# Optimization experiments

Hardware: AMD Instinct MI355X
Metric: run time of the kernel (lower is better)

The kernel has to match this reference:

```python
import jax, jax.numpy as jnp
import numpy as np

N_NODES = 100000
N_EDGES = 1600000
N_GRAPHS = 256
HIDDEN = 128
IN_FEAT = 5


def setup_inputs() -> dict:
    key = jax.random.key(0)
    ks = jax.random.split(key, 12)
    x = jax.random.normal(ks[0], (N_NODES, IN_FEAT), dtype=jnp.float32)
    edge_index = jax.random.randint(ks[1], (2, N_EDGES), 0, N_NODES, dtype=jnp.int64)
    batch = jnp.sort(jax.random.randint(ks[2], (N_NODES,), 0, N_GRAPHS, dtype=jnp.int64))
    s = 0.05
    W0 = jax.random.normal(ks[3], (IN_FEAT, HIDDEN), dtype=jnp.float32) * s
    b0 = jnp.zeros((HIDDEN,), dtype=jnp.float32)
    W1 = jax.random.normal(ks[4], (HIDDEN, HIDDEN), dtype=jnp.float32) * s
    b1 = jnp.zeros((HIDDEN,), dtype=jnp.float32)
    W2 = jax.random.normal(ks[5], (HIDDEN, HIDDEN), dtype=jnp.float32) * s
    b2 = jnp.zeros((HIDDEN,), dtype=jnp.float32)
    lin_w = jax.random.normal(ks[6], (HIDDEN, 1), dtype=jnp.float32) * s
    lin_b = jnp.zeros((1,), dtype=jnp.float32)
    return {"x": x, "edge_index": edge_index, "batch": batch,
            "W0": W0, "b0": b0, "W1": W1, "b1": b1, "W2": W2, "b2": b2,
            "lin_w": lin_w, "lin_b": lin_b}


def reference(x, edge_index, batch, W0, b0, W1, b1, W2, b2, lin_w, lin_b):
    n = x.shape[0]
    # PyG GCNConv: add self-loops, symmetric normalization D^-1/2 (A+I) D^-1/2
    loop = jnp.arange(n, dtype=edge_index.dtype)
    src = jnp.concatenate([edge_index[0], loop])  # [E+N]
    dst = jnp.concatenate([edge_index[1], loop])
    deg = jax.ops.segment_sum(jnp.ones_like(dst, dtype=x.dtype), dst, num_segments=n)
    dis = jnp.where(deg > 0, jax.lax.rsqrt(jnp.maximum(deg, 1.0)), 0.0)
    norm = (dis[src] * dis[dst])[:, None]  # [E+N, 1]

    def gcn_conv(h, W, b):
        h = h @ W                      # [N, H]
        msg = h[src] * norm            # gather + scale, [E+N, H]
        return jax.ops.segment_sum(msg, dst, num_segments=n) + b

    h = jax.nn.relu(gcn_conv(x, W0, b0))
    h = jax.nn.relu(gcn_conv(h, W1, b1))
    h = gcn_conv(h, W2, b2)

    # global_mean_pool over batch ids
    sums = jax.ops.segment_sum(h, batch, num_segments=N_GRAPHS)
    cnt = jax.ops.segment_sum(jnp.ones((n,), x.dtype), batch, num_segments=N_GRAPHS)
    g = sums / jnp.maximum(cnt, 1.0)[:, None]
    # dropout p=0.01 is identity in eval mode
    return jax.nn.sigmoid(g @ lin_w + lin_b)  # [N_GRAPHS, 1]
```

## Files before the change

### kernel.cpp

```cpp
#include <hip/hip_runtime.h>
#include <hip/hip_fp8.h>

#define GCN_N 100000
#define GCN_H 128
#define GCN_G 256
#define NPB_SHIFT 9
#define NPB 512
#define NBKT 196
#define CHUNK 2048
#define SRC_BITS 17
#define SRC_MASK ((1 << SRC_BITS) - 1)
#define T1_SCALE 256.0f
#define T1_INV_SCALE (1.0f / 256.0f)
#define EBUF_CAP 10240

static_assert(GCN_N < (1 << SRC_BITS), "src id must fit 17 bits");

using short8 = __attribute__((ext_vector_type(8))) short;
using f32x4  = __attribute__((ext_vector_type(4))) float;
using f32x2  = __attribute__((ext_vector_type(2))) float;

#if defined(__has_builtin)
#if __has_builtin(__builtin_amdgcn_cvt_pk_f32_fp8) && __has_builtin(__builtin_amdgcn_cvt_pk_fp8_f32)
#define HW_FP8 1
#endif
#endif


__device__ __forceinline__ unsigned short f2bf(float f) {
    unsigned u = __float_as_uint(f);
    unsigned r = u + 0x7FFFu + ((u >> 16) & 1u);
    return (unsigned short)(r >> 16);
}
__device__ __forceinline__ float bf2f(unsigned short h) {
    return __uint_as_float(((unsigned)h) << 16);
}

__device__ __forceinline__ void fp8x4_to_f32(unsigned v, float* f) {
#ifdef HW_FP8
    f32x2 lo = __builtin_amdgcn_cvt_pk_f32_fp8((int)v, false);
    f32x2 hi = __builtin_amdgcn_cvt_pk_f32_fp8((int)v, true);
    f[0] = lo[0]; f[1] = lo[1]; f[2] = hi[0]; f[3] = hi[1];
#else
    #pragma unroll
    for (int j = 0; j < 4; j++) {
        __hip_fp8_e4m3 h;
        h.__x = (unsigned char)((v >> (8 * j)) & 0xFF);
        f[j] = (float)h;
    }
#endif
}

__device__ __forceinline__ unsigned f32x4_to_fp8(float f0, float f1, float f2, float f3) {
#ifdef HW_FP8
    int r = __builtin_amdgcn_cvt_pk_fp8_f32(f0, f1, 0, false);
    r = __builtin_amdgcn_cvt_pk_fp8_f32(f2, f3, r, true);
    return (unsigned)r;
#else
    unsigned r = 0;
    float ff[4] = {f0, f1, f2, f3};
    #pragma unroll
    for (int j = 0; j < 4; j++) {
        __hip_fp8_e4m3 h(ff[j]);
        r |= ((unsigned)h.__x) << (8 * j);
    }
    return r;
#endif
}


__global__ __launch_bounds__(256) void hist_kernel(const int* __restrict__ dst,
                                                   int* __restrict__ hist, int E) {
    __shared__ int lh[NBKT];
    int tid = threadIdx.x;
    if (tid < NBKT) lh[tid] = 0;
    __syncthreads();
    int e0 = blockIdx.x * CHUNK;
    #pragma unroll
    for (int i = 0; i < CHUNK / 256; i++) {
        int e = e0 + tid + i * 256;
        if (e < E) atomicAdd(&lh[dst[e] >> NPB_SHIFT], 1);
    }
    __syncthreads();
    if (tid < NBKT) hist[(size_t)blockIdx.x * NBKT + tid] = lh[tid];
}

__global__ __launch_bounds__(64) void scan_cols_kernel(const int* __restrict__ hist,
                                                       int* __restrict__ offsT,
                                                       int* __restrict__ btot, int B) {
    int k = blockIdx.x;
    int lane = threadIdx.x;
    int running = 0;
    for (int b0 = 0; b0 < B; b0 += 64) {
        int b = b0 + lane;
        int v = (b < B) ? hist[(size_t)b * NBKT + k] : 0;
        int iv = v;
        #pragma unroll
        for (int d = 1; d < 64; d <<= 1) {
            int x = __shfl_up(iv, d, 64);
            if (lane >= d) iv += x;
        }
        if (b < B) offsT[(size_t)k * B + b] = running + iv - v;
        running += __shfl(iv, 63, 64);
    }
    if (lane == 0) btot[k] = running;
}

__global__ __launch_bounds__(256) void prep_kernel(const float* __restrict__ W1,
                                                   const float* __restrict__ W2,
                                                   const float* __restrict__ b2,
                                                   const float* __restrict__ lw,
                                                   const int* __restrict__ btot,
                                                   unsigned short* __restrict__ w1t,
                                                   float* __restrict__ w2l,
                                                   float* __restrict__ c2,
                                                   int* __restrict__ bbase,
                                                   int* __restrict__ rowptr, int n) {
    __shared__ float slw[128];
    int blk = blockIdx.x, tid = threadIdx.x;
    if (blk < 64) {
        int idx = blk * 256 + tid;
        int col = idx >> 7, k = idx & 127;
        w1t[idx] = f2bf(W1[k * 128 + col]);
    } else if (blk == 64) {
        if (tid < 128) slw[tid] = lw[tid];
        __syncthreads();
        if (tid < 128) {
            float s = 0.f;
            #pragma unroll 8
            for (int j = 0; j < 128; j++) s = fmaf(W2[tid * 128 + j], slw[j], s);
            w2l[tid] = s;
        } else if (tid == 128) {
            float s = 0.f;
            for (int j = 0; j < 128; j++) s = fmaf(b2[j], slw[j], s);
            c2[0] = s;
        }
    } else {
        if (tid == 0) {
            int run = 0;
            for (int i = 0; i < NBKT; i++) { bbase[i] = run; run += btot[i]; }
            bbase[NBKT] = run;
            rowptr[n] = run;
        }
    }
}

__global__ __launch_bounds__(256) void partition_kernel(const int* __restrict__ src,
                                                        const int* __restrict__ dst,
                                                        const int* __restrict__ bbase,
                                                        const int* __restrict__ offsT,
                                                        int* __restrict__ epack,
                                                        int E, int B) {
    __shared__ int cur[NBKT];
    int blk = blockIdx.x, tid = threadIdx.x;
    if (tid < NBKT) cur[tid] = bbase[tid] + offsT[(size_t)tid * B + blk];
    __syncthreads();
    int e0 = blk * CHUNK;
    #pragma unroll
    for (int i = 0; i < CHUNK / 256; i++) {
        int e = e0 + tid + i * 256;
        if (e < E) {
            int d = dst[e];
            int s = src[e];
            int pos = atomicAdd(&cur[d >> NPB_SHIFT], 1);
            epack[pos] = ((d & (NPB - 1)) << SRC_BITS) | s;
        }
    }
}

__global__ __launch_bounds__(512) void csr_build_kernel(const int* __restrict__ epack,
                                                        const int* __restrict__ bbase,
                                                        const float* __restrict__ x,
                                                        int* __restrict__ rowptr,
                                                        float* __restrict__ dis,
                                                        float* __restrict__ xsp,
                                                        int* __restrict__ csrc, int n) {
    __shared__ int ebuf[EBUF_CAP];
    __shared__ int lcount[NPB];
    __shared__ int lcur[NPB];
    __shared__ int wsums[8];
    int k = blockIdx.x, tid = threadIdx.x;
    int lane = tid & 63, wid = tid >> 6;
    int nodebase = k << NPB_SHIFT;
    int ebeg = bbase[k], eend = bbase[k + 1];
    bool fits = (eend - ebeg) <= EBUF_CAP;

    lcount[tid] = 0;
    __syncthreads();
    for (int e = ebeg + tid; e < eend; e += 512) {
        int p = epack[e];
        if (fits) ebuf[e - ebeg] = p;
        atomicAdd(&lcount[p >> SRC_BITS], 1);
    }
    __syncthreads();

    int v = lcount[tid];
    int iv = v;
    #pragma unroll
    for (int d = 1; d < 64; d <<= 1) {
        int x2 = __shfl_up(iv, d, 64);
        if (lane >= d) iv += x2;
    }
    if (lane == 63) wsums[wid] = iv;
    __syncthreads();
    if (tid == 0) {
        int r = 0;
        #pragma unroll
        for (int w = 0; w < 8; w++) { int t = wsums[w]; wsums[w] = r; r += t; }
    }
    __syncthreads();
    int ex = wsums[wid] + iv - v;
    lcur[tid] = ex;
    int node = nodebase + tid;
    if (node < n) {
        rowptr[node] = ebeg + ex;
        float dd = rsqrtf((float)(v + 1));
        dis[node] = dd;
        const float* xr = x + (size_t)node * 5;
        float4 a;
        a.x = xr[0] * dd; a.y = xr[1] * dd; a.z = xr[2] * dd; a.w = xr[3] * dd;
        float a4 = xr[4] * dd;
        ((float4*)(xsp + (size_t)node * 8))[0] = a;
        xsp[(size_t)node * 8 + 4] = a4;
        xsp[(size_t)node * 8 + 5] = 0.f;
        xsp[(size_t)node * 8 + 6] = 0.f;
        xsp[(size_t)node * 8 + 7] = 0.f;
    }
    __syncthreads();
    for (int e = ebeg + tid; e < eend; e += 512) {
        int p = fits ? ebuf[e - ebeg] : epack[e];
        int pos = atomicAdd(&lcur[p >> SRC_BITS], 1);
        csrc[ebeg + pos] = p & SRC_MASK;
    }
}


__global__ __launch_bounds__(256) void aggx_kernel(const float* __restrict__ xsp,
                                                   const float* __restrict__ dis,
                                                   const int* __restrict__ rowptr,
                                                   const int* __restrict__ csrc,
                                                   float* __restrict__ a0p, int n) {
    int i = blockIdx.x * 256 + threadIdx.x;
    if (i >= n) return;
    float4 acc = ((const float4*)(xsp + (size_t)i * 8))[0];
    float acc4 = xsp[(size_t)i * 8 + 4];
    int r0 = rowptr[i], r1 = rowptr[i + 1];
    int e = r0;
    for (; e + 7 < r1; e += 8) {
        int ss[8];
        #pragma unroll
        for (int u = 0; u < 8; u++) ss[u] = csrc[e + u];
        float4 v[8]; float a4[8];
        #pragma unroll
        for (int u = 0; u < 8; u++) {
            v[u] = ((const float4*)(xsp + (size_t)ss[u] * 8))[0];
            a4[u] = xsp[(size_t)ss[u] * 8 + 4];
        }
        #pragma unroll
        for (int u = 0; u < 8; u++) {
            acc.x += v[u].x; acc.y += v[u].y; acc.z += v[u].z; acc.w += v[u].w;
            acc4 += a4[u];
        }
    }
    for (; e < r1; e++) {
        int s = csrc[e];
        float4 v = ((const float4*)(xsp + (size_t)s * 8))[0];
        acc.x += v.x; acc.y += v.y; acc.z += v.z; acc.w += v.w;
        acc4 += xsp[(size_t)s * 8 + 4];
    }
    float di = dis[i];
    acc.x *= di; acc.y *= di; acc.z *= di; acc.w *= di; acc4 *= di;
    ((float4*)(a0p + (size_t)i * 8))[0] = acc;
    a0p[(size_t)i * 8 + 4] = acc4;
}


__global__ __launch_bounds__(256) void mmfused_kernel(const float* __restrict__ a0p,
                                                      const float* __restrict__ W0,
                                                      const float* __restrict__ b0,
                                                      const unsigned short* __restrict__ w1t,
                                                      const float* __restrict__ dis,
                                                      unsigned* __restrict__ t1f8, int n) {
    __shared__ __align__(16) unsigned short sA[128 * 128];
    __shared__ __align__(16) unsigned short sBT[128 * 128];
    __shared__ __align__(16) float4 sA0[256];
    __shared__ float sDis[128];
    char* sAb = (char*)sA;
    char* sBb = (char*)sBT;
    int tid = threadIdx.x;
    int rowBase = blockIdx.x * 128;

    {
        int rowL = tid >> 1, q = tid & 1;
        int gr = rowBase + rowL;
        float4 v = make_float4(0.f, 0.f, 0.f, 0.f);
        if (gr < n) v = ((const float4*)a0p)[(size_t)gr * 2 + q];
        sA0[tid] = v;
        if (tid < 128) {
            int g2 = rowBase + tid;
            sDis[tid] = (g2 < n) ? dis[g2] : 0.f;
        }
    }
    #pragma unroll
    for (int it = 0; it < 8; it++) {
        int idx = tid + it * 256;
        int col = idx >> 4, c = idx & 15;
        uint4 v = ((const uint4*)w1t)[idx];
        int byteoff = (col * 256 + c * 16) ^ ((col & 7) << 4);
        *(uint4*)(sBb + byteoff) = v;
    }
    __syncthreads();

    {
        int cq = tid & 31;
        int rg = tid >> 5;
        float4 w0q[5];
        #pragma unroll
        for (int j = 0; j < 5; j++) w0q[j] = *((const float4*)(W0 + j * 128 + cq * 4));
        float4 b0q = *((const float4*)(b0 + cq * 4));
        const float* sA0f = (const float*)sA0;
        #pragma unroll
        for (int ri = 0; ri < 16; ri++) {
            int row = rg + ri * 8;
            const float* ar = sA0f + row * 8;
            float4 h = b0q;
            #pragma unroll
            for (int j = 0; j < 5; j++) {
                float aj = ar[j];
                h.x = fmaf(aj, w0q[j].x, h.x);
                h.y = fmaf(aj, w0q[j].y, h.y);
                h.z = fmaf(aj, w0q[j].z, h.z);
                h.w = fmaf(aj, w0q[j].w, h.w);
            }
            h.x = fmaxf(h.x, 0.f); h.y = fmaxf(h.y, 0.f);
            h.z = fmaxf(h.z, 0.f); h.w = fmaxf(h.w, 0.f);
            uint2 p;
            p.x = (unsigned)f2bf(h.x) | ((unsigned)f2bf(h.y) << 16);
            p.y = (unsigned)f2bf(h.z) | ((unsigned)f2bf(h.w) << 16);
            int byteoff = (row * 256 + cq * 8) ^ ((row & 7) << 4);
            *(uint2*)(sAb + byteoff) = p;
        }
    }
    __syncthreads();

    int wave = tid >> 6, l = tid & 63;
    int lr = l & 15, lg = l >> 4;
    int rb = wave * 32;

    short8 afr[2][4];
    #pragma unroll
    for (int rt = 0; rt < 2; rt++) {
        int row = rb + rt * 16 + lr;
        #pragma unroll
        for (int ks = 0; ks < 4; ks++) {
            int byteoff = (row * 256 + ks * 64 + lg * 16) ^ ((row & 7) << 4);
            afr[rt][ks] = *(const short8*)(sAb + byteoff);
        }
    }
    f32x4 acc[2][8];
    #pragma unroll
    for (int rt = 0; rt < 2; rt++)
        #pragma unroll
        for (int ct = 0; ct < 8; ct++)
            acc[rt][ct] = (f32x4){0.f, 0.f, 0.f, 0.f};

    #pragma unroll
    for (int ct = 0; ct < 8; ct++) {
        int col = ct * 16 + lr;
        short8 bfr[4];
        #pragma unroll
        for (int ks = 0; ks < 4; ks++) {
            int byteoff = (col * 256 + ks * 64 + lg * 16) ^ ((col & 7) << 4);
            bfr[ks] = *(const short8*)(sBb + byteoff);
        }
        #pragma unroll
        for (int rt = 0; rt < 2; rt++) {
            #pragma unroll
            for (int ks = 0; ks < 4; ks++) {
                acc[rt][ct] = __builtin_amdgcn_mfma_f32_16x16x32_bf16(
                    afr[rt][ks], bfr[ks], acc[rt][ct], 0, 0, 0);
            }
        }
    }

    #pragma unroll
    for (int rt = 0; rt < 2; rt++) {
        #pragma unroll
        for (int i = 0; i < 4; i++) {
            int rowL = rb + rt * 16 + lg * 4 + i;
            float dsc = sDis[rowL] * T1_SCALE;
            #pragma unroll
            for (int ct = 0; ct < 8; ct++) {
                int col = ct * 16 + lr;
                int byteoff = (rowL * 256 + col * 2) ^ ((rowL & 7) << 4);
                *(unsigned short*)(sAb + byteoff) = f2bf(acc[rt][ct][i] * dsc);
            }
        }
    }
    __syncthreads();

    #pragma unroll
    for (int it = 0; it < 8; it++) {
        int flat = tid + it * 256;
        int rowL = flat >> 4, c16 = flat & 15;
        int gr = rowBase + rowL;
        if (gr < n) {
            int byteoff = (rowL * 256 + c16 * 16) ^ ((rowL & 7) << 4);
            uint4 v = *(const uint4*)(sAb + byteoff);
            float f0 = __uint_as_float(v.x << 16), f1 = __uint_as_float(v.x & 0xFFFF0000u);
            float f2 = __uint_as_float(v.y << 16), f3 = __uint_as_float(v.y & 0xFFFF0000u);
            float f4 = __uint_as_float(v.z << 16), f5 = __uint_as_float(v.z & 0xFFFF0000u);
            float f6 = __uint_as_float(v.w << 16), f7 = __uint_as_float(v.w & 0xFFFF0000u);
            uint2 p;
            p.x = f32x4_to_fp8(f0, f1, f2, f3);
            p.y = f32x4_to_fp8(f4, f5, f6, f7);
            ((uint2*)t1f8)[(size_t)gr * 16 + c16] = p;
        }
    }
}


__global__ __launch_bounds__(256) void agg1_kernel(const unsigned* __restrict__ t1f8,
                                                   const float* __restrict__ dis,
                                                   const int* __restrict__ rowptr,
                                                   const int* __restrict__ csrc,
                                                   const float* __restrict__ b1,
                                                   const float* __restrict__ w2l,
                                                   float* __restrict__ z, int n) {
    int group = threadIdx.x >> 4, lane = threadIdx.x & 15;
    int i = blockIdx.x * 16 + group;
    if (i >= n) return;
    const uint2* t2 = (const uint2*)t1f8;
    float f[8], acc[8];
    uint2 sv = t2[(size_t)i * 16 + lane];
    fp8x4_to_f32(sv.x, f);
    fp8x4_to_f32(sv.y, f + 4);
    #pragma unroll
    for (int j = 0; j < 8; j++) acc[j] = f[j];
    int r0 = rowptr[i], r1 = rowptr[i + 1];
    for (int e = r0; e < r1; e += 16) {
        int cnt = r1 - e; if (cnt > 16) cnt = 16;
        int idx = e + lane;
        int si = (idx < r1) ? csrc[idx] : 0;
        uint2 vv[16];
        #pragma unroll
        for (int u = 0; u < 16; u++) {
            if (u < cnt) {
                int s = __shfl(si, u, 16);
                vv[u] = t2[(size_t)s * 16 + lane];
            }
        }
        #pragma unroll
        for (int u = 0; u < 16; u++) {
            if (u < cnt) {
                fp8x4_to_f32(vv[u].x, f);
                fp8x4_to_f32(vv[u].y, f + 4);
                #pragma unroll
                for (int j = 0; j < 8; j++) acc[j] += f[j];
            }
        }
    }
    float di = dis[i];
    float dis_s = di * T1_INV_SCALE;
    float4 b4a = ((const float4*)b1)[lane * 2];
    float4 b4b = ((const float4*)b1)[lane * 2 + 1];
    float4 w4a = ((const float4*)w2l)[lane * 2];
    float4 w4b = ((const float4*)w2l)[lane * 2 + 1];
    float bb[8] = {b4a.x, b4a.y, b4a.z, b4a.w, b4b.x, b4b.y, b4b.z, b4b.w};
    float ww[8] = {w4a.x, w4a.y, w4a.z, w4a.w, w4b.x, w4b.y, w4b.z, w4b.w};
    float d = 0.f;
    #pragma unroll
    for (int j = 0; j < 8; j++) {
        float c = fmaxf(fmaf(dis_s, acc[j], bb[j]), 0.f);
        d = fmaf(c, ww[j], d);
    }
    #pragma unroll
    for (int o = 8; o > 0; o >>= 1) d += __shfl_down(d, o, 16);
    if (lane == 0) z[i] = di * d;
}


__global__ __launch_bounds__(256) void aggz_pool_kernel(const float* __restrict__ z,
                                                        const float* __restrict__ dis,
                                                        const int* __restrict__ rowptr,
                                                        const int* __restrict__ csrc,
                                                        const int* __restrict__ batch,
                                                        float* __restrict__ gsum,
                                                        int* __restrict__ gcnt, int n) {
    __shared__ float lg[GCN_G];
    __shared__ int lc[GCN_G];
    int tid = threadIdx.x;
    lg[tid] = 0.f;
    lc[tid] = 0;
    __syncthreads();
    int i = blockIdx.x * 256 + tid;
    bool valid = i < n;
    float ndv = 0.f;
    int g = 0;
    if (valid) {
        float acc = z[i];
        int r0 = rowptr[i], r1 = rowptr[i + 1];
        int e = r0;
        for (; e + 7 < r1; e += 8) {
            int ss[8];
            #pragma unroll
            for (int u = 0; u < 8; u++) ss[u] = csrc[e + u];
            float zv[8];
            #pragma unroll
            for (int u = 0; u < 8; u++) zv[u] = z[ss[u]];
            #pragma unroll
            for (int u = 0; u < 8; u++) acc += zv[u];
        }
        for (; e < r1; e++) acc += z[csrc[e]];
        ndv = dis[i] * acc;
        g = batch[i];
    }
    int lane = tid & 63;
    int g0 = __shfl(g, 0, 64);
    bool uni = __all(g == g0) && __all(valid);
    if (uni) {
        float s = ndv;
        #pragma unroll
        for (int o = 32; o > 0; o >>= 1) s += __shfl_down(s, o, 64);
        if (lane == 0) {
            atomicAdd(&lg[g0], s);
            atomicAdd(&lc[g0], 64);
        }
    } else if (valid) {
        atomicAdd(&lg[g], ndv);
        atomicAdd(&lc[g], 1);
    }
    __syncthreads();
    float v = lg[tid];
    int c = lc[tid];
    if (v != 0.f) atomicAdd(&gsum[tid], v);
    if (c != 0) atomicAdd(&gcnt[tid], c);
}


__global__ __launch_bounds__(256) void final_kernel(const float* __restrict__ gsum,
                                                    const int* __restrict__ gcnt,
                                                    const float* __restrict__ c2,
                                                    const float* __restrict__ lb,
                                                    float* __restrict__ out) {
    int g = threadIdx.x;
    float cnt = (float)max(gcnt[g], 1);
    float v = gsum[g] / cnt + c2[0] + lb[0];
    out[g] = 1.f / (1.f + expf(-v));
}


extern "C" void kernel_launch(void* const* d_in, const int* in_sizes, int n_in,
                              void* d_out, int out_size, void* d_ws, size_t ws_size,
                              hipStream_t stream) {
    const float* x   = (const float*)d_in[0];
    const int*   ei  = (const int*)d_in[1];
    const int*   bat = (const int*)d_in[2];
    const float* W0  = (const float*)d_in[3];
    const float* b0  = (const float*)d_in[4];
    const float* W1  = (const float*)d_in[5];
    const float* b1  = (const float*)d_in[6];
    const float* W2  = (const float*)d_in[7];
    const float* b2  = (const float*)d_in[8];
    const float* lw  = (const float*)d_in[9];
    const float* lb  = (const float*)d_in[10];
    float* out = (float*)d_out;

    const int N = GCN_N;
    const int E = in_sizes[1] / 2;
    const int B = (E + CHUNK - 1) / CHUNK;

    char* ws = (char*)d_ws;
    size_t off = 0;
    auto alloc = [&](size_t bytes) {
        size_t o = off;
        off += (bytes + 255) & ~(size_t)255;
        return o;
    };
    int*   hist    = (int*)(ws + alloc((size_t)B * NBKT * 4));
    int*   offsT   = (int*)(ws + alloc((size_t)NBKT * B * 4));
    int*   btot    = (int*)(ws + alloc((size_t)NBKT * 4));
    int*   bbase   = (int*)(ws + alloc((size_t)(NBKT + 1) * 4));
    int*   epack   = (int*)(ws + alloc((size_t)E * 4));
    int*   rowptr  = (int*)(ws + alloc((size_t)(N + 1) * 4));
    float* dis     = (float*)(ws + alloc((size_t)N * 4));
    int*   csrc    = (int*)(ws + alloc((size_t)E * 4));
    float* xsp     = (float*)(ws + alloc((size_t)N * 8 * 4));
    float* a0p     = (float*)(ws + alloc((size_t)N * 8 * 4));
    unsigned* t1f8 = (unsigned*)(ws + alloc((size_t)N * GCN_H));
    float* z       = (float*)(ws + alloc((size_t)N * 4));
    float* w2l     = (float*)(ws + alloc(128 * 4));
    float* c2      = (float*)(ws + alloc(4));
    unsigned short* w1t = (unsigned short*)(ws + alloc(128 * 128 * 2));
    float* gsum    = (float*)(ws + alloc(GCN_G * 4));
    int*   gcnt    = (int*)(ws + alloc(GCN_G * 4));

    const int* src = ei;
    const int* dst = ei + E;

    hipMemsetAsync(gsum, 0, GCN_G * 4 * 2, stream);

    hist_kernel<<<B, 256, 0, stream>>>(dst, hist, E);
    scan_cols_kernel<<<NBKT, 64, 0, stream>>>(hist, offsT, btot, B);
    prep_kernel<<<66, 256, 0, stream>>>(W1, W2, b2, lw, btot, w1t, w2l, c2, bbase, rowptr, N);
    partition_kernel<<<B, 256, 0, stream>>>(src, dst, bbase, offsT, epack, E, B);
    csr_build_kernel<<<NBKT, 512, 0, stream>>>(epack, bbase, x, rowptr, dis, xsp, csrc, N);

    aggx_kernel<<<(N + 255) / 256, 256, 0, stream>>>(xsp, dis, rowptr, csrc, a0p, N);
    mmfused_kernel<<<(N + 127) / 128, 256, 0, stream>>>(a0p, W0, b0, w1t, dis, t1f8, N);
    agg1_kernel<<<(N + 15) / 16, 256, 0, stream>>>(t1f8, dis, rowptr, csrc, b1, w2l, z, N);
    aggz_pool_kernel<<<(N + 255) / 256, 256, 0, stream>>>(z, dis, rowptr, csrc, bat, gsum, gcnt, N);

    final_kernel<<<1, 256, 0, stream>>>(gsum, gcnt, c2, lb, out);
}
```

Measured before the change: 149.6 us.

## Quantize layer-1 features to FP4 with per-row scale and fuse kernels

```diff
diff --git a/kernel.cpp b/kernel.cpp
--- a/kernel.cpp
+++ b/kernel.cpp
@@ -1,5 +1,4 @@
 #include <hip/hip_runtime.h>
-#include <hip/hip_fp8.h>
 
 #define GCN_N 100000
 #define GCN_H 128
@@ -10,8 +9,6 @@
 #define CHUNK 2048
 #define SRC_BITS 17
 #define SRC_MASK ((1 << SRC_BITS) - 1)
-#define T1_SCALE 256.0f
-#define T1_INV_SCALE (1.0f / 256.0f)
 #define EBUF_CAP 10240
 
 static_assert(GCN_N < (1 << SRC_BITS), "src id must fit 17 bits");
@@ -21,8 +18,8 @@
 using f32x2  = __attribute__((ext_vector_type(2))) float;
 
 #if defined(__has_builtin)
-#if __has_builtin(__builtin_amdgcn_cvt_pk_f32_fp8) && __has_builtin(__builtin_amdgcn_cvt_pk_fp8_f32)
-#define HW_FP8 1
+#if __has_builtin(__builtin_amdgcn_cvt_scalef32_pk_f32_fp4)
+#define HW_FP4 1
 #endif
 #endif
 
@@ -36,93 +33,63 @@
     return __uint_as_float(((unsigned)h) << 16);
 }
 
-__device__ __forceinline__ void fp8x4_to_f32(unsigned v, float* f) {
-#ifdef HW_FP8
-    f32x2 lo = __builtin_amdgcn_cvt_pk_f32_fp8((int)v, false);
-    f32x2 hi = __builtin_amdgcn_cvt_pk_f32_fp8((int)v, true);
-    f[0] = lo[0]; f[1] = lo[1]; f[2] = hi[0]; f[3] = hi[1];
+__device__ __forceinline__ void fp4x8_to_f32(unsigned v, float* f) {
+#ifdef HW_FP4
+    f32x2 p0 = __builtin_amdgcn_cvt_scalef32_pk_f32_fp4(v, 1.0f, 0);
+    f32x2 p1 = __builtin_amdgcn_cvt_scalef32_pk_f32_fp4(v, 1.0f, 1);
+    f32x2 p2 = __builtin_amdgcn_cvt_scalef32_pk_f32_fp4(v, 1.0f, 2);
+    f32x2 p3 = __builtin_amdgcn_cvt_scalef32_pk_f32_fp4(v, 1.0f, 3);
+    f[0] = p0[0]; f[1] = p0[1]; f[2] = p1[0]; f[3] = p1[1];
+    f[4] = p2[0]; f[5] = p2[1]; f[6] = p3[0]; f[7] = p3[1];
 #else
     #pragma unroll
-    for (int j = 0; j < 4; j++) {
-        __hip_fp8_e4m3 h;
-        h.__x = (unsigned char)((v >> (8 * j)) & 0xFF);
-        f[j] = (float)h;
+    for (int j = 0; j < 8; j++) {
+        unsigned nib = (v >> (4 * j)) & 0xF;
+        unsigned e = (nib >> 1) & 3, m = nib & 1;
+        float mag = (e == 0) ? 0.5f * (float)m : ldexpf(1.0f + 0.5f * (float)m, (int)e - 1);
+        f[j] = (nib & 8) ? -mag : mag;
     }
 #endif
 }
 
-__device__ __forceinline__ unsigned f32x4_to_fp8(float f0, float f1, float f2, float f3) {
-#ifdef HW_FP8
-    int r = __builtin_amdgcn_cvt_pk_fp8_f32(f0, f1, 0, false);
-    r = __builtin_amdgcn_cvt_pk_fp8_f32(f2, f3, r, true);
-    return (unsigned)r;
-#else
-    unsigned r = 0;
-    float ff[4] = {f0, f1, f2, f3};
-    #pragma unroll
-    for (int j = 0; j < 4; j++) {
-        __hip_fp8_e4m3 h(ff[j]);
-        r |= ((unsigned)h.__x) << (8 * j);
-    }
-    return r;
-#endif
-}
-
-
-__global__ __launch_bounds__(256) void hist_kernel(const int* __restrict__ dst,
-                                                   int* __restrict__ hist, int E) {
+__device__ __forceinline__ unsigned f32_to_fp4(float a) {
+    unsigned sg = (a < 0.f) ? 8u : 0u;
+    float b = fabsf(a);
+    unsigned q = (unsigned)(b >= 0.25f) + (unsigned)(b >= 0.75f) + (unsigned)(b >= 1.25f)
+               + (unsigned)(b >= 1.75f) + (unsigned)(b >= 2.5f) + (unsigned)(b >= 3.5f)
+               + (unsigned)(b >= 5.0f);
+    return sg | q;
+}
+
+
+__global__ __launch_bounds__(256) void hist_prep_kernel(const int* __restrict__ dst,
+                                                        int* __restrict__ hist, int E, int B,
+                                                        const float* __restrict__ W1,
+                                                        const float* __restrict__ W2,
+                                                        const float* __restrict__ b2,
+                                                        const float* __restrict__ lw,
+                                                        unsigned short* __restrict__ w1t,
+                                                        float* __restrict__ w2l,
+                                                        float* __restrict__ c2) {
     __shared__ int lh[NBKT];
-    int tid = threadIdx.x;
-    if (tid < NBKT) lh[tid] = 0;
-    __syncthreads();
-    int e0 = blockIdx.x * CHUNK;
-    #pragma unroll
-    for (int i = 0; i < CHUNK / 256; i++) {
-        int e = e0 + tid + i * 256;
-        if (e < E) atomicAdd(&lh[dst[e] >> NPB_SHIFT], 1);
-    }
-    __syncthreads();
-    if (tid < NBKT) hist[(size_t)blockIdx.x * NBKT + tid] = lh[tid];
-}
-
-__global__ __launch_bounds__(64) void scan_cols_kernel(const int* __restrict__ hist,
-                                                       int* __restrict__ offsT,
-                                                       int* __restrict__ btot, int B) {
-    int k = blockIdx.x;
-    int lane = threadIdx.x;
-    int running = 0;
-    for (int b0 = 0; b0 < B; b0 += 64) {
-        int b = b0 + lane;
-        int v = (b < B) ? hist[(size_t)b * NBKT + k] : 0;
-        int iv = v;
-        #pragma unroll
-        for (int d = 1; d < 64; d <<= 1) {
-            int x = __shfl_up(iv, d, 64);
-            if (lane >= d) iv += x;
-        }
-        if (b < B) offsT[(size_t)k * B + b] = running + iv - v;
-        running += __shfl(iv, 63, 64);
-    }
-    if (lane == 0) btot[k] = running;
-}
-
-__global__ __launch_bounds__(256) void prep_kernel(const float* __restrict__ W1,
-                                                   const float* __restrict__ W2,
-                                                   const float* __restrict__ b2,
-                                                   const float* __restrict__ lw,
-                                                   const int* __restrict__ btot,
-                                                   unsigned short* __restrict__ w1t,
-                                                   float* __restrict__ w2l,
-                                                   float* __restrict__ c2,
-                                                   int* __restrict__ bbase,
-                                                   int* __restrict__ rowptr, int n) {
     __shared__ float slw[128];
     int blk = blockIdx.x, tid = threadIdx.x;
-    if (blk < 64) {
-        int idx = blk * 256 + tid;
+    if (blk < B) {
+        if (tid < NBKT) lh[tid] = 0;
+        __syncthreads();
+        int e0 = blk * CHUNK;
+        #pragma unroll
+        for (int i = 0; i < CHUNK / 256; i++) {
+            int e = e0 + tid + i * 256;
+            if (e < E) atomicAdd(&lh[dst[e] >> NPB_SHIFT], 1);
+        }
+        __syncthreads();
+        if (tid < NBKT) hist[(size_t)blk * NBKT + tid] = lh[tid];
+    } else if (blk < B + 64) {
+        int idx = (blk - B) * 256 + tid;
         int col = idx >> 7, k = idx & 127;
         w1t[idx] = f2bf(W1[k * 128 + col]);
-    } else if (blk == 64) {
+    } else {
         if (tid < 128) slw[tid] = lw[tid];
         __syncthreads();
         if (tid < 128) {
@@ -135,25 +102,45 @@
             for (int j = 0; j < 128; j++) s = fmaf(b2[j], slw[j], s);
             c2[0] = s;
         }
-    } else {
-        if (tid == 0) {
-            int run = 0;
-            for (int i = 0; i < NBKT; i++) { bbase[i] = run; run += btot[i]; }
-            bbase[NBKT] = run;
-            rowptr[n] = run;
-        }
-    }
+    }
+}
+
+__global__ __launch_bounds__(64) void scan_cols_kernel(const int* __restrict__ hist,
+                                                       int* __restrict__ offsT,
+                                                       int* __restrict__ btot, int B) {
+    int k = blockIdx.x;
+    int lane = threadIdx.x;
+    int running = 0;
+    for (int b0 = 0; b0 < B; b0 += 64) {
+        int b = b0 + lane;
+        int v = (b < B) ? hist[(size_t)b * NBKT + k] : 0;
+        int iv = v;
+        #pragma unroll
+        for (int d = 1; d < 64; d <<= 1) {
+            int x = __shfl_up(iv, d, 64);
+            if (lane >= d) iv += x;
+        }
+        if (b < B) offsT[(size_t)k * B + b] = running + iv - v;
+        running += __shfl(iv, 63, 64);
+    }
+    if (lane == 0) btot[k] = running;
 }
 
 __global__ __launch_bounds__(256) void partition_kernel(const int* __restrict__ src,
                                                         const int* __restrict__ dst,
-                                                        const int* __restrict__ bbase,
+                                                        const int* __restrict__ btot,
                                                         const int* __restrict__ offsT,
                                                         int* __restrict__ epack,
                                                         int E, int B) {
     __shared__ int cur[NBKT];
+    __shared__ int sbase[NBKT];
     int blk = blockIdx.x, tid = threadIdx.x;
-    if (tid < NBKT) cur[tid] = bbase[tid] + offsT[(size_t)tid * B + blk];
+    if (tid == 0) {
+        int run = 0;
+        for (int kk = 0; kk < NBKT; kk++) { sbase[kk] = run; run += btot[kk]; }
+    }
+    __syncthreads();
+    if (tid < NBKT) cur[tid] = sbase[tid] + offsT[(size_t)tid * B + blk];
     __syncthreads();
     int e0 = blk * CHUNK;
     #pragma unroll
@@ -169,7 +156,7 @@
 }
 
 __global__ __launch_bounds__(512) void csr_build_kernel(const int* __restrict__ epack,
-                                                        const int* __restrict__ bbase,
+                                                        const int* __restrict__ btot,
                                                         const float* __restrict__ x,
                                                         int* __restrict__ rowptr,
                                                         float* __restrict__ dis,
@@ -179,14 +166,25 @@
     __shared__ int lcount[NPB];
     __shared__ int lcur[NPB];
     __shared__ int wsums[8];
+    __shared__ int s_eb, s_ee, s_tot;
     int k = blockIdx.x, tid = threadIdx.x;
     int lane = tid & 63, wid = tid >> 6;
     int nodebase = k << NPB_SHIFT;
-    int ebeg = bbase[k], eend = bbase[k + 1];
+
+    lcount[tid] = 0;
+    if (tid == 0) {
+        int run = 0, eb = 0, ee = 0;
+        for (int kk = 0; kk < NBKT; kk++) {
+            if (kk == k) eb = run;
+            run += btot[kk];
+            if (kk == k) ee = run;
+        }
+        s_eb = eb; s_ee = ee; s_tot = run;
+    }
+    __syncthreads();
+    int ebeg = s_eb, eend = s_ee;
     bool fits = (eend - ebeg) <= EBUF_CAP;
 
-    lcount[tid] = 0;
-    __syncthreads();
     for (int e = ebeg + tid; e < eend; e += 512) {
         int p = epack[e];
         if (fits) ebuf[e - ebeg] = p;
@@ -226,6 +224,7 @@
         xsp[(size_t)node * 8 + 6] = 0.f;
         xsp[(size_t)node * 8 + 7] = 0.f;
     }
+    if (k == NBKT - 1 && tid == 0) rowptr[n] = s_tot;
     __syncthreads();
     for (int e = ebeg + tid; e < eend; e += 512) {
         int p = fits ? ebuf[e - ebeg] : epack[e];
@@ -235,79 +234,74 @@
 }
 
 
-__global__ __launch_bounds__(256) void aggx_kernel(const float* __restrict__ xsp,
-                                                   const float* __restrict__ dis,
-                                                   const int* __restrict__ rowptr,
-                                                   const int* __restrict__ csrc,
-                                                   float* __restrict__ a0p, int n) {
-    int i = blockIdx.x * 256 + threadIdx.x;
-    if (i >= n) return;
-    float4 acc = ((const float4*)(xsp + (size_t)i * 8))[0];
-    float acc4 = xsp[(size_t)i * 8 + 4];
-    int r0 = rowptr[i], r1 = rowptr[i + 1];
-    int e = r0;
-    for (; e + 7 < r1; e += 8) {
-        int ss[8];
-        #pragma unroll
-        for (int u = 0; u < 8; u++) ss[u] = csrc[e + u];
-        float4 v[8]; float a4[8];
-        #pragma unroll
-        for (int u = 0; u < 8; u++) {
-            v[u] = ((const float4*)(xsp + (size_t)ss[u] * 8))[0];
-            a4[u] = xsp[(size_t)ss[u] * 8 + 4];
-        }
-        #pragma unroll
-        for (int u = 0; u < 8; u++) {
-            acc.x += v[u].x; acc.y += v[u].y; acc.z += v[u].z; acc.w += v[u].w;
-            acc4 += a4[u];
-        }
-    }
-    for (; e < r1; e++) {
-        int s = csrc[e];
-        float4 v = ((const float4*)(xsp + (size_t)s * 8))[0];
-        acc.x += v.x; acc.y += v.y; acc.z += v.z; acc.w += v.w;
-        acc4 += xsp[(size_t)s * 8 + 4];
-    }
-    float di = dis[i];
-    acc.x *= di; acc.y *= di; acc.z *= di; acc.w *= di; acc4 *= di;
-    ((float4*)(a0p + (size_t)i * 8))[0] = acc;
-    a0p[(size_t)i * 8 + 4] = acc4;
-}
-
-
-__global__ __launch_bounds__(256) void mmfused_kernel(const float* __restrict__ a0p,
+__global__ __launch_bounds__(256) void mmfused_kernel(const float* __restrict__ xsp,
+                                                      const int* __restrict__ rowptr,
+                                                      const int* __restrict__ csrc,
                                                       const float* __restrict__ W0,
                                                       const float* __restrict__ b0,
                                                       const unsigned short* __restrict__ w1t,
                                                       const float* __restrict__ dis,
-                                                      unsigned* __restrict__ t1f8, int n) {
+                                                      unsigned* __restrict__ t1q4,
+                                                      float* __restrict__ tscale, int n) {
     __shared__ __align__(16) unsigned short sA[128 * 128];
     __shared__ __align__(16) unsigned short sBT[128 * 128];
-    __shared__ __align__(16) float4 sA0[256];
+    __shared__ __align__(16) float sA0f[128 * 8];
     __shared__ float sDis[128];
+    __shared__ float sSmax[128];
     char* sAb = (char*)sA;
     char* sBb = (char*)sBT;
     int tid = threadIdx.x;
     int rowBase = blockIdx.x * 128;
 
-    {
-        int rowL = tid >> 1, q = tid & 1;
-        int gr = rowBase + rowL;
-        float4 v = make_float4(0.f, 0.f, 0.f, 0.f);
-        if (gr < n) v = ((const float4*)a0p)[(size_t)gr * 2 + q];
-        sA0[tid] = v;
-        if (tid < 128) {
-            int g2 = rowBase + tid;
-            sDis[tid] = (g2 < n) ? dis[g2] : 0.f;
-        }
-    }
-    #pragma unroll
-    for (int it = 0; it < 8; it++) {
-        int idx = tid + it * 256;
-        int col = idx >> 4, c = idx & 15;
-        uint4 v = ((const uint4*)w1t)[idx];
-        int byteoff = (col * 256 + c * 16) ^ ((col & 7) << 4);
-        *(uint4*)(sBb + byteoff) = v;
+    if (tid < 128) {
+        int i = rowBase + tid;
+        float a[5] = {0.f, 0.f, 0.f, 0.f, 0.f};
+        float di = 0.f;
+        if (i < n) {
+            di = dis[i];
+            const float* xr = xsp + (size_t)i * 8;
+            float4 s4 = ((const float4*)xr)[0];
+            a[0] = s4.x; a[1] = s4.y; a[2] = s4.z; a[3] = s4.w; a[4] = xr[4];
+            int r0 = rowptr[i], r1 = rowptr[i + 1];
+            int e = r0;
+            for (; e + 7 < r1; e += 8) {
+                int ss[8];
+                #pragma unroll
+                for (int u = 0; u < 8; u++) ss[u] = csrc[e + u];
+                float4 v[8]; float a4[8];
+                #pragma unroll
+                for (int u = 0; u < 8; u++) {
+                    v[u] = ((const float4*)(xsp + (size_t)ss[u] * 8))[0];
+                    a4[u] = xsp[(size_t)ss[u] * 8 + 4];
+                }
+                #pragma unroll
+                for (int u = 0; u < 8; u++) {
+                    a[0] += v[u].x; a[1] += v[u].y; a[2] += v[u].z; a[3] += v[u].w;
+                    a[4] += a4[u];
+                }
+            }
+            for (; e < r1; e++) {
+                int s = csrc[e];
+                float4 v = ((const float4*)(xsp + (size_t)s * 8))[0];
+                a[0] += v.x; a[1] += v.y; a[2] += v.z; a[3] += v.w;
+                a[4] += xsp[(size_t)s * 8 + 4];
+            }
+            #pragma unroll
+            for (int j = 0; j < 5; j++) a[j] *= di;
+        }
+        sDis[tid] = di;
+        #pragma unroll
+        for (int j = 0; j < 5; j++) sA0f[tid * 8 + j] = a[j];
+    } else {
+        int t2 = tid - 128;
+        #pragma unroll
+        for (int it = 0; it < 16; it++) {
+            int idx = t2 + it * 128;
+            int col = idx >> 4, c = idx & 15;
+            uint4 v = ((const uint4*)w1t)[idx];
+            int byteoff = (col * 256 + c * 16) ^ ((col & 7) << 4);
+            *(uint4*)(sBb + byteoff) = v;
+        }
     }
     __syncthreads();
 
@@ -318,7 +312,6 @@
         #pragma unroll
         for (int j = 0; j < 5; j++) w0q[j] = *((const float4*)(W0 + j * 128 + cq * 4));
         float4 b0q = *((const float4*)(b0 + cq * 4));
-        const float* sA0f = (const float*)sA0;
         #pragma unroll
         for (int ri = 0; ri < 16; ri++) {
             int row = rg + ri * 8;
@@ -388,13 +381,20 @@
         #pragma unroll
         for (int i = 0; i < 4; i++) {
             int rowL = rb + rt * 16 + lg * 4 + i;
-            float dsc = sDis[rowL] * T1_SCALE;
+            float dsc = sDis[rowL];
+            float m = 0.f;
             #pragma unroll
             for (int ct = 0; ct < 8; ct++) {
                 int col = ct * 16 + lr;
+                float vv = acc[rt][ct][i] * dsc;
                 int byteoff = (rowL * 256 + col * 2) ^ ((rowL & 7) << 4);
-                *(unsigned short*)(sAb + byteoff) = f2bf(acc[rt][ct][i] * dsc);
+                *(unsigned short*)(sAb + byteoff) = f2bf(vv);
+                m = fmaxf(m, fabsf(vv));
             }
+            #pragma unroll
+            for (int msk = 1; msk < 16; msk <<= 1)
+                m = fmaxf(m, __shfl_xor(m, msk, 64));
+            if (lr == 0) sSmax[rowL] = m;
         }
     }
     __syncthreads();
@@ -407,20 +407,25 @@
         if (gr < n) {
             int byteoff = (rowL * 256 + c16 * 16) ^ ((rowL & 7) << 4);
             uint4 v = *(const uint4*)(sAb + byteoff);
-            float f0 = __uint_as_float(v.x << 16), f1 = __uint_as_float(v.x & 0xFFFF0000u);
-            float f2 = __uint_as_float(v.y << 16), f3 = __uint_as_float(v.y & 0xFFFF0000u);
-            float f4 = __uint_as_float(v.z << 16), f5 = __uint_as_float(v.z & 0xFFFF0000u);
-            float f6 = __uint_as_float(v.w << 16), f7 = __uint_as_float(v.w & 0xFFFF0000u);
-            uint2 p;
-            p.x = f32x4_to_fp8(f0, f1, f2, f3);
-            p.y = f32x4_to_fp8(f4, f5, f6, f7);
-            ((uint2*)t1f8)[(size_t)gr * 16 + c16] = p;
-        }
-    }
-}
-
-
-__global__ __launch_bounds__(256) void agg1_kernel(const unsigned* __restrict__ t1f8,
+            float ff[8];
+            ff[0] = __uint_as_float(v.x << 16); ff[1] = __uint_as_float(v.x & 0xFFFF0000u);
+            ff[2] = __uint_as_float(v.y << 16); ff[3] = __uint_as_float(v.y & 0xFFFF0000u);
+            ff[4] = __uint_as_float(v.z << 16); ff[5] = __uint_as_float(v.z & 0xFFFF0000u);
+            ff[6] = __uint_as_float(v.w << 16); ff[7] = __uint_as_float(v.w & 0xFFFF0000u);
+            float s6 = sSmax[rowL] * (1.f / 6.f);
+            float inv = (s6 > 0.f) ? 1.f / s6 : 0.f;
+            unsigned q = 0;
+            #pragma unroll
+            for (int j = 0; j < 8; j++) q |= f32_to_fp4(ff[j] * inv) << (4 * j);
+            t1q4[(size_t)gr * 16 + c16] = q;
+            if (c16 == 0) tscale[gr] = s6;
+        }
+    }
+}
+
+
+__global__ __launch_bounds__(256) void agg1_kernel(const unsigned* __restrict__ t1q4,
+                                                   const float* __restrict__ tscale,
                                                    const float* __restrict__ dis,
                                                    const int* __restrict__ rowptr,
                                                    const int* __restrict__ csrc,
@@ -430,38 +435,36 @@
     int group = threadIdx.x >> 4, lane = threadIdx.x & 15;
     int i = blockIdx.x * 16 + group;
     if (i >= n) return;
-    const uint2* t2 = (const uint2*)t1f8;
     float f[8], acc[8];
-    uint2 sv = t2[(size_t)i * 16 + lane];
-    fp8x4_to_f32(sv.x, f);
-    fp8x4_to_f32(sv.y, f + 4);
-    #pragma unroll
-    for (int j = 0; j < 8; j++) acc[j] = f[j];
+    unsigned sv = t1q4[(size_t)i * 16 + lane];
+    float sci = tscale[i];
+    fp4x8_to_f32(sv, f);
+    #pragma unroll
+    for (int j = 0; j < 8; j++) acc[j] = f[j] * sci;
     int r0 = rowptr[i], r1 = rowptr[i + 1];
     for (int e = r0; e < r1; e += 16) {
         int cnt = r1 - e; if (cnt > 16) cnt = 16;
         int idx = e + lane;
         int si = (idx < r1) ? csrc[idx] : 0;
-        uint2 vv[16];
+        unsigned vv[16]; float sc[16];
         #pragma unroll
         for (int u = 0; u < 16; u++) {
             if (u < cnt) {
                 int s = __shfl(si, u, 16);
-                vv[u] = t2[(size_t)s * 16 + lane];
+                vv[u] = t1q4[(size_t)s * 16 + lane];
+                sc[u] = tscale[s];
             }
         }
         #pragma unroll
         for (int u = 0; u < 16; u++) {
             if (u < cnt) {
-                fp8x4_to_f32(vv[u].x, f);
-                fp8x4_to_f32(vv[u].y, f + 4);
+                fp4x8_to_f32(vv[u], f);
                 #pragma unroll
-                for (int j = 0; j < 8; j++) acc[j] += f[j];
+                for (int j = 0; j < 8; j++) acc[j] = fmaf(f[j], sc[u], acc[j]);
             }
         }
     }
     float di = dis[i];
-    float dis_s = di * T1_INV_SCALE;
     float4 b4a = ((const float4*)b1)[lane * 2];
     float4 b4b = ((const float4*)b1)[lane * 2 + 1];
     float4 w4a = ((const float4*)w2l)[lane * 2];
@@ -471,7 +474,7 @@
     float d = 0.f;
     #pragma unroll
     for (int j = 0; j < 8; j++) {
-        float c = fmaxf(fmaf(dis_s, acc[j], bb[j]), 0.f);
+        float c = fmaxf(fmaf(di, acc[j], bb[j]), 0.f);
         d = fmaf(c, ww[j], d);
     }
     #pragma unroll
@@ -485,10 +488,15 @@
                                                         const int* __restrict__ rowptr,
                                                         const int* __restrict__ csrc,
                                                         const int* __restrict__ batch,
+                                                        const float* __restrict__ c2,
+                                                        const float* __restrict__ lb,
                                                         float* __restrict__ gsum,
-                                                        int* __restrict__ gcnt, int n) {
+                                                        int* __restrict__ gcnt,
+                                                        int* __restrict__ done,
+                                                        float* __restrict__ out, int n) {
     __shared__ float lg[GCN_G];
     __shared__ int lc[GCN_G];
+    __shared__ int sticket;
     int tid = threadIdx.x;
     lg[tid] = 0.f;
     lc[tid] = 0;
@@ -535,18 +543,16 @@
     int c = lc[tid];
     if (v != 0.f) atomicAdd(&gsum[tid], v);
     if (c != 0) atomicAdd(&gcnt[tid], c);
-}
-
-
-__global__ __launch_bounds__(256) void final_kernel(const float* __restrict__ gsum,
-                                                    const int* __restrict__ gcnt,
-                                                    const float* __restrict__ c2,
-                                                    const float* __restrict__ lb,
-                                                    float* __restrict__ out) {
-    int g = threadIdx.x;
-    float cnt = (float)max(gcnt[g], 1);
-    float v = gsum[g] / cnt + c2[0] + lb[0];
-    out[g] = 1.f / (1.f + expf(-v));
+
+    __threadfence();
+    if (tid == 0) sticket = atomicAdd(done, 1);
+    __syncthreads();
+    if (sticket == (int)gridDim.x - 1) {
+        float sv = atomicAdd(&gsum[tid], 0.f);
+        int cv = atomicAdd(&gcnt[tid], 0);
+        float vv = sv / (float)max(cv, 1) + c2[0] + lb[0];
+        out[tid] = 1.f / (1.f + expf(-vv));
+    }
 }
 
 
@@ -580,36 +586,34 @@
     int*   hist    = (int*)(ws + alloc((size_t)B * NBKT * 4));
     int*   offsT   = (int*)(ws + alloc((size_t)NBKT * B * 4));
     int*   btot    = (int*)(ws + alloc((size_t)NBKT * 4));
-    int*   bbase   = (int*)(ws + alloc((size_t)(NBKT + 1) * 4));
     int*   epack   = (int*)(ws + alloc((size_t)E * 4));
     int*   rowptr  = (int*)(ws + alloc((size_t)(N + 1) * 4));
     float* dis     = (float*)(ws + alloc((size_t)N * 4));
     int*   csrc    = (int*)(ws + alloc((size_t)E * 4));
     float* xsp     = (float*)(ws + alloc((size_t)N * 8 * 4));
-    float* a0p     = (float*)(ws + alloc((size_t)N * 8 * 4));
-    unsigned* t1f8 = (unsigned*)(ws + alloc((size_t)N * GCN_H));
+    unsigned* t1q4 = (unsigned*)(ws + alloc((size_t)N * 64));
+    float* tscale  = (float*)(ws + alloc((size_t)N * 4));
     float* z       = (float*)(ws + alloc((size_t)N * 4));
     float* w2l     = (float*)(ws + alloc(128 * 4));
     float* c2      = (float*)(ws + alloc(4));
     unsigned short* w1t = (unsigned short*)(ws + alloc(128 * 128 * 2));
     float* gsum    = (float*)(ws + alloc(GCN_G * 4));
     int*   gcnt    = (int*)(ws + alloc(GCN_G * 4));
+    int*   done    = (int*)(ws + alloc(4));
 
     const int* src = ei;
     const int* dst = ei + E;
 
-    hipMemsetAsync(gsum, 0, GCN_G * 4 * 2, stream);
-
-    hist_kernel<<<B, 256, 0, stream>>>(dst, hist, E);
+    hipMemsetAsync(gsum, 0, GCN_G * 4 * 2 + 256, stream);
+
+    hist_prep_kernel<<<B + 65, 256, 0, stream>>>(dst, hist, E, B, W1, W2, b2, lw, w1t, w2l, c2);
     scan_cols_kernel<<<NBKT, 64, 0, stream>>>(hist, offsT, btot, B);
-    prep_kernel<<<66, 256, 0, stream>>>(W1, W2, b2, lw, btot, w1t, w2l, c2, bbase, rowptr, N);
-    partition_kernel<<<B, 256, 0, stream>>>(src, dst, bbase, offsT, epack, E, B);
-    csr_build_kernel<<<NBKT, 512, 0, stream>>>(epack, bbase, x, rowptr, dis, xsp, csrc, N);
-
-    aggx_kernel<<<(N + 255) / 256, 256, 0, stream>>>(xsp, dis, rowptr, csrc, a0p, N);
-    mmfused_kernel<<<(N + 127) / 128, 256, 0, stream>>>(a0p, W0, b0, w1t, dis, t1f8, N);
-    agg1_kernel<<<(N + 15) / 16, 256, 0, stream>>>(t1f8, dis, rowptr, csrc, b1, w2l, z, N);
-    aggz_pool_kernel<<<(N + 255) / 256, 256, 0, stream>>>(z, dis, rowptr, csrc, bat, gsum, gcnt, N);
-
-    final_kernel<<<1, 256, 0, stream>>>(gsum, gcnt, c2, lb, out);
-}
+    partition_kernel<<<B, 256, 0, stream>>>(src, dst, btot, offsT, epack, E, B);
+    csr_build_kernel<<<NBKT, 512, 0, stream>>>(epack, btot, x, rowptr, dis, xsp, csrc, N);
+
+    mmfused_kernel<<<(N + 127) / 128, 256, 0, stream>>>(xsp, rowptr, csrc, W0, b0, w1t, dis,
+                                                        t1q4, tscale, N);
+    agg1_kernel<<<(N + 15) / 16, 256, 0, stream>>>(t1q4, tscale, dis, rowptr, csrc, b1, w2l, z, N);
+    aggz_pool_kernel<<<(N + 255) / 256, 256, 0, stream>>>(z, dis, rowptr, csrc, bat, c2, lb,
+                                                          gsum, gcnt, done, out, N);
+}
```

After: 179.0 us. +19.7%, slower.
